# Kernel tuning notes

Hardware: AMD Instinct MI355X
Metric: run time of the kernel (lower is better)

The kernel has to match this reference:

```python
import jax, jax.numpy as jnp
import numpy as np

KH = KW = 3
PAD = 1
OFFG = 8  # offset groups: 144 offset channels / (2*9)


def conv2d(x, w, b, pad=PAD):
    out = jax.lax.conv_general_dilated(
        x, w, window_strides=(1, 1), padding=[(pad, pad), (pad, pad)],
        dimension_numbers=('NCHW', 'OIHW', 'NCHW'))
    return out + b[None, :, None, None]


def deform_conv2d(x, offset, w, b):
    # x: [B,C,H,W], offset: [B, 2*K*OFFG, H, W] (per group: (y,x) per kernel tap)
    B, C, H, W = x.shape
    K = KH * KW
    Cg = C // OFFG
    off = offset.reshape(B, OFFG, K, 2, H, W)
    ky, kx = jnp.meshgrid(jnp.arange(KH), jnp.arange(KW), indexing='ij')
    ky = ky.reshape(K).astype(x.dtype)
    kx = kx.reshape(K).astype(x.dtype)
    ys = (jnp.arange(H) - PAD).astype(x.dtype)  # stride 1, dilation 1
    xs = (jnp.arange(W) - PAD).astype(x.dtype)
    # sampling positions [B, OFFG, K, H, W]
    py = ys[None, None, None, :, None] + ky[None, None, :, None, None] + off[:, :, :, 0]
    px = xs[None, None, None, None, :] + kx[None, None, :, None, None] + off[:, :, :, 1]
    y0 = jnp.floor(py)
    x0 = jnp.floor(px)
    xg = x.reshape(B, OFFG, Cg, H * W)
    cols = jnp.zeros((B, OFFG, Cg, K, H, W), x.dtype)
    for dy in (0, 1):
        for dx in (0, 1):
            yi = y0 + dy
            xi = x0 + dx
            wgt = (1.0 - jnp.abs(py - yi)) * (1.0 - jnp.abs(px - xi))
            valid = (yi >= 0) & (yi < H) & (xi >= 0) & (xi < W)
            yc = jnp.clip(yi, 0, H - 1).astype(jnp.int32)
            xc = jnp.clip(xi, 0, W - 1).astype(jnp.int32)
            idx = (yc * W + xc).reshape(B, OFFG, 1, K * H * W)
            g = jnp.take_along_axis(xg, idx, axis=3).reshape(B, OFFG, Cg, K, H, W)
            cols = cols + g * (wgt * valid.astype(x.dtype))[:, :, None]
    cols = cols.reshape(B, C, K, H, W)
    out = jnp.einsum('bckhw,ock->bohw', cols, w.reshape(w.shape[0], C, K))
    return out + b[None, :, None, None]


def setup_inputs() -> dict:
    key = jax.random.key(0)
    ks = jax.random.split(key, 6)
    B, C, H, W = 16, 144, 64, 64
    feat_arm = jax.random.normal(ks[0], (B, C, H, W), jnp.float32)
    feat_up = jax.random.normal(ks[1], (B, C, H, W), jnp.float32)
    # offset conv: in=288 (cat), out=144 = 2*9*OFFG; small init so offsets are sane
    off_w = jax.random.normal(ks[2], (144, 288, 3, 3), jnp.float32) * 0.01
    off_b = jnp.zeros((144,), jnp.float32)
    dcn_w = jax.random.normal(ks[3], (256, 144, 3, 3), jnp.float32) * (1.0 / np.sqrt(144 * 9))
    dcn_b = jnp.zeros((256,), jnp.float32)
    return {'feat_arm': feat_arm, 'feat_up': feat_up, 'off_w': off_w,
            'off_b': off_b, 'dcn_w': dcn_w, 'dcn_b': dcn_b}


def reference(feat_arm, feat_up, off_w, off_b, dcn_w, dcn_b):
    x = jnp.concatenate([feat_arm, feat_up], axis=1)  # [B, 288, H, W]
    offset = conv2d(x, off_w, off_b)                  # [B, 144, H, W]
    y = deform_conv2d(feat_up, offset, dcn_w, dcn_b)  # [B, 256, H, W]
    return jax.nn.silu(y)
```

## Files before the change

### kernel.cpp

```cpp
#include <hip/hip_runtime.h>
#include <math.h>

constexpr int BN = 16;
constexpr int C_IN = 144, C_CAT = 288, C_OFF = 144, C_OUT = 256;
constexpr int OFFG = 8, CG = 18;

constexpr int FUB_ELEMS  = C_IN * BN * 4096;
constexpr int OFFP_ELEMS = BN * 72 * 4096;
constexpr int WOFF_PACK = 9 * 9 * 9 * 512;
constexpr int WDCN_PACK = 8 * 6 * 16 * 512;

typedef __attribute__((ext_vector_type(8))) short bf16x8;
typedef __attribute__((ext_vector_type(4))) float f32x4;
typedef __attribute__((ext_vector_type(2))) _Float16 f16x2;
typedef __attribute__((ext_vector_type(4))) unsigned u32x4;

__device__ __forceinline__ unsigned short f2bf(float f) {
  unsigned u = __builtin_bit_cast(unsigned, f);
  return (unsigned short)((u + 0x7FFFu + ((u >> 16) & 1u)) >> 16);
}

__device__ __forceinline__ unsigned packh2(float a, float b) {
  unsigned short ha = __builtin_bit_cast(unsigned short, (_Float16)a);
  unsigned short hb = __builtin_bit_cast(unsigned short, (_Float16)b);
  return (unsigned)ha | ((unsigned)hb << 16);
}
__device__ __forceinline__ float h2f_lo(unsigned u) {
  return (float)__builtin_bit_cast(_Float16, (unsigned short)(u & 0xFFFFu));
}
__device__ __forceinline__ float h2f_hi(unsigned u) {
  return (float)__builtin_bit_cast(_Float16, (unsigned short)(u >> 16));
}
__device__ __forceinline__ float bf_lo(unsigned u) {
  return __builtin_bit_cast(float, u << 16);
}
__device__ __forceinline__ float bf_hi(unsigned u) {
  return __builtin_bit_cast(float, u & 0xFFFF0000u);
}

__device__ __forceinline__ void gload_lds16(const void* g, void* l) {
  __builtin_amdgcn_global_load_lds(
      (const __attribute__((address_space(1))) unsigned*)g,
      (__attribute__((address_space(3))) unsigned*)l, 16, 0, 0);
}

__global__ __launch_bounds__(256) void tobf16_fu(
    const float* __restrict__ fu, unsigned short* __restrict__ fuB) {
  int i = (blockIdx.x * 256 + threadIdx.x) * 4;
  float4 v = *(const float4*)(fu + i);
  ushort4 o;
  o.x = f2bf(v.x); o.y = f2bf(v.y); o.z = f2bf(v.z); o.w = f2bf(v.w);
  *(ushort4*)(fuB + i) = o;
}

__global__ __launch_bounds__(256) void pack_w(
    const float* __restrict__ off_w, const float* __restrict__ dcn_w,
    unsigned short* __restrict__ wo, unsigned short* __restrict__ wd) {
  int idx = blockIdx.x * 256 + threadIdx.x;
  if (idx < WOFF_PACK) {
    int i = idx & 7, lane = (idx >> 3) & 63, t = idx >> 9;
    int mt = t % 9; t /= 9;
    int tap = t % 9, cb = t / 9;
    int co = mt * 16 + (lane & 15);
    int ci = cb * 32 + ((lane >> 4) << 3) + i;
    wo[idx] = f2bf(off_w[(co * C_CAT + ci) * 9 + tap]);
  }
  if (idx < WDCN_PACK) {
    int i = idx & 7, lane = (idx >> 3) & 63, t = idx >> 9;
    int mt = t & 15; t >>= 4;
    int ks = t % 6, g = t / 6;
    int co = mt * 16 + (lane & 15);
    int r = ks * 32 + ((lane >> 4) << 3) + i;
    float v = 0.f;
    if (r < 162) {
      int ci = r / 9, tap = r - ci * 9;
      v = dcn_w[(co * C_IN + g * CG + ci) * 9 + tap];
    }
    wd[idx] = f2bf(v);
  }
}

__global__ __launch_bounds__(256) void offs_conv_mfma(
    const float* __restrict__ fa, const float* __restrict__ fu,
    const unsigned short* __restrict__ wt, const float* __restrict__ bias,
    unsigned* __restrict__ offp) {
  const int b = blockIdx.x >> 5;
  const int y0 = (blockIdx.x & 31) << 1;
  const int tid = threadIdx.x;
  const int wave = tid >> 6, lane = tid & 63;
  const int kg = lane >> 4, ln = lane & 15;

  __shared__ __align__(16) unsigned short xs[4 * 66 * 32];

  f32x4 acc[9][2];
#pragma unroll
  for (int m = 0; m < 9; ++m)
#pragma unroll
    for (int n = 0; n < 2; ++n) acc[m][n] = {0.f, 0.f, 0.f, 0.f};

  for (int cb = 0; cb < 9; ++cb) {
    __syncthreads();
    for (int idx = tid; idx < 2112; idx += 256) {
      int q = idx / 264;
      int rem = idx - q * 264;
      int row = rem / 66;
      int cc = rem - row * 66;
      int y = y0 - 1 + row, x = cc - 1;
      ushort4 wv = make_ushort4(0, 0, 0, 0);
      if (y >= 0 && y < 64 && x >= 0 && x < 64) {
        int cib = cb * 32 + (q << 2);
        const float* p = (cib < C_IN)
                             ? fa + (((size_t)(b * C_IN + cib)) << 12)
                             : fu + (((size_t)(b * C_IN + cib - C_IN)) << 12);
        int o = (y << 6) + x;
        wv.x = f2bf(p[o]);
        wv.y = f2bf(p[o + 4096]);
        wv.z = f2bf(p[o + 8192]);
        wv.w = f2bf(p[o + 12288]);
      }
      int e = ((row * 66 + cc) << 5) + (((q >> 1) ^ (cc & 3)) << 3) + ((q & 1) << 2);
      *(ushort4*)&xs[e] = wv;
    }
    __syncthreads();

    for (int tap = 0; tap < 9; ++tap) {
      const int ky = tap / 3, kx = tap - ky * 3;
      bf16x8 a[9];
      const unsigned short* wp = wt + (((size_t)(cb * 9 + tap) * 9) << 9) + (lane << 3);
#pragma unroll
      for (int m = 0; m < 9; ++m) a[m] = *(const bf16x8*)(wp + (m << 9));
#pragma unroll
      for (int n = 0; n < 2; ++n) {
        int px = ((wave << 1) + n) * 16 + ln;
        int row = (px >> 6) + ky, cc = (px & 63) + kx;
        int e = ((row * 66 + cc) << 5) + ((kg ^ (cc & 3)) << 3);
        bf16x8 bv = *(const bf16x8*)&xs[e];
#pragma unroll
        for (int m = 0; m < 9; ++m)
          acc[m][n] = __builtin_amdgcn_mfma_f32_16x16x32_bf16(a[m], bv, acc[m][n], 0, 0, 0);
      }
    }
  }

#pragma unroll
  for (int n = 0; n < 2; ++n) {
    int px = ((wave << 1) + n) * 16 + ln;
    int y = y0 + (px >> 6), x = px & 63;
#pragma unroll
    for (int m = 0; m < 9; ++m) {
      int cob = m * 16 + (kg << 2);
#pragma unroll
      for (int rr = 0; rr < 4; rr += 2) {
        unsigned v = packh2(acc[m][n][rr] + bias[cob + rr],
                            acc[m][n][rr + 1] + bias[cob + rr + 1]);
        offp[(((size_t)(b * 72 + ((cob + rr) >> 1))) << 12) + (y << 6) + x] = v;
      }
    }
  }
}

__global__ __launch_bounds__(512, 4) void dcn_mfma(
    const unsigned short* __restrict__ fuB, const unsigned* __restrict__ offp,
    const unsigned short* __restrict__ wt, const float* __restrict__ bias,
    float* __restrict__ out) {
  const int b = blockIdx.x >> 6, h = blockIdx.x & 63;
  const int tid = threadIdx.x;
  const int wave = tid >> 6, lane = tid & 63;
  const int kg = lane >> 4, ln = lane & 15;
  const int wm = wave >> 2, wn = wave & 3;
  const int px = (wn << 4) + ln;

  __shared__ __align__(16) unsigned short colsT[64 * 202];
  __shared__ __align__(16) unsigned short wl[2][8192];

  f32x4 acc[8];
#pragma unroll
  for (int m = 0; m < 8; ++m) acc[m] = {0.f, 0.f, 0.f, 0.f};

  for (int i = tid; i < 64 * 15; i += 512) {
    int p = i / 15, d = i - p * 15;
    *(unsigned*)&colsT[p * 202 + 162 + 2 * d] = 0u;
  }

  {
    const unsigned short* src = wt + (wave * 2) * 512 + lane * 8;
#pragma unroll
    for (int j = 0; j < 2; ++j)
      gload_lds16(src + j * 512, &wl[0][(wave * 2 + j) * 512]);
  }

  auto make_geo = [&](int gg_, int tap, int p) -> uint4 {
    int ky = tap / 3, kx = tap - ky * 3;
    unsigned op = offp[(((size_t)(b * 72 + gg_ * 9 + tap)) << 12) + (h << 6) + p];
    float oy = h2f_lo(op), ox = h2f_hi(op);
    float py = (float)(h - 1 + ky) + oy;
    float pxs = (float)(p - 1 + kx) + ox;
    float y0f = floorf(py), x0f = floorf(pxs);
    int y0 = (int)y0f, x0 = (int)x0f;
    float fy = py - y0f, fx = pxs - x0f;
    float vy0 = (y0 >= 0 && y0 < 64) ? 1.f : 0.f;
    float vy1 = (y0 + 1 >= 0 && y0 + 1 < 64) ? 1.f : 0.f;
    float vx0 = (x0 >= 0 && x0 < 64) ? 1.f : 0.f;
    float vx1 = (x0 + 1 >= 0 && x0 + 1 < 64) ? 1.f : 0.f;
    float a0 = (1.f - fx) * vx0;
    float a1 = fx * vx1;
    float wlo = (x0 == -1) ? a1 : (x0 == 63 ? 0.f : a0);
    float whi = (x0 == 63) ? a0 : (x0 == -1 ? 0.f : a1);
    int xL = min(max(x0, 0), 62);
    int yc0 = min(max(y0, 0), 63), yc1 = min(max(y0 + 1, 0), 63);
    float cy0 = (1.f - fy) * vy0, cy1 = fy * vy1;
    uint4 r;
    r.x = (unsigned)((yc0 << 6) + xL) | ((unsigned)((yc1 << 6) + xL) << 16);
    r.y = 0u;
    r.z = packh2(cy0 * wlo, cy0 * whi);
    r.w = packh2(cy1 * wlo, cy1 * whi);
    return r;
  };

  int t = 0;
  for (int g = 0; g < OFFG; ++g) {
    __syncthreads();

    uint4 gg = make_geo(g, wave, lane);
    uint4 g8 = make_geo(g, 8, lane);

    const unsigned short* gbase = fuB + (((size_t)(b * C_IN + g * CG)) << 12);
    {
      const int iL0 = gg.x & 0xFFFFu, iL1 = gg.x >> 16;
      const float wl0 = h2f_lo(gg.z), wh0 = h2f_hi(gg.z);
      const float wl1 = h2f_lo(gg.w), wh1 = h2f_hi(gg.w);
      for (int cb = 0; cb < 18; cb += 6) {
        unsigned d0[6], d1[6];
#pragma unroll
        for (int u = 0; u < 6; ++u) {
          const unsigned short* pl = gbase + ((size_t)(cb + u) << 12);
          __builtin_memcpy(&d0[u], pl + iL0, 4);
          __builtin_memcpy(&d1[u], pl + iL1, 4);
        }
#pragma unroll
        for (int u = 0; u < 6; ++u) {
          float s = wl0 * bf_lo(d0[u]) + wh0 * bf_hi(d0[u]) +
                    wl1 * bf_lo(d1[u]) + wh1 * bf_hi(d1[u]);
          colsT[lane * 202 + (cb + u) * 9 + wave] = f2bf(s);
        }
      }
      const int j0 = g8.x & 0xFFFFu, j1 = g8.x >> 16;
      const float ul0 = h2f_lo(g8.z), uh0 = h2f_hi(g8.z);
      const float ul1 = h2f_lo(g8.w), uh1 = h2f_hi(g8.w);
      const int n8 = (wave < 2) ? 3 : 2;
      unsigned e0[3], e1[3];
#pragma unroll
      for (int u = 0; u < 3; ++u) {
        if (u < n8) {
          const unsigned short* pl = gbase + ((size_t)(wave + 8 * u) << 12);
          __builtin_memcpy(&e0[u], pl + j0, 4);
          __builtin_memcpy(&e1[u], pl + j1, 4);
        }
      }
#pragma unroll
      for (int u = 0; u < 3; ++u) {
        if (u < n8) {
          float s = ul0 * bf_lo(e0[u]) + uh0 * bf_hi(e0[u]) +
                    ul1 * bf_lo(e1[u]) + uh1 * bf_hi(e1[u]);
          colsT[lane * 202 + (wave + 8 * u) * 9 + 8] = f2bf(s);
        }
      }
    }
    __syncthreads();

    for (int ks = 0; ks < 6; ++ks, ++t) {
      int cbase = px * 202 + ks * 32 + (kg << 3);
      u32x4 bu;
      bu[0] = *(const unsigned*)&colsT[cbase];
      bu[1] = *(const unsigned*)&colsT[cbase + 2];
      bu[2] = *(const unsigned*)&colsT[cbase + 4];
      bu[3] = *(const unsigned*)&colsT[cbase + 6];
      bf16x8 bv = __builtin_bit_cast(bf16x8, bu);

      __syncthreads();

      if (t < 47) {
        const unsigned short* src =
            wt + (size_t)(t + 1) * 8192 + (wave * 2) * 512 + lane * 8;
        unsigned short* dst = wl[(t + 1) & 1];
#pragma unroll
        for (int j = 0; j < 2; ++j)
          gload_lds16(src + j * 512, dst + (wave * 2 + j) * 512);
      }

      const unsigned short* wbuf = wl[t & 1] + (wm * 8) * 512 + lane * 8;
#pragma unroll
      for (int j = 0; j < 8; ++j) {
        bf16x8 av = *(const bf16x8*)(wbuf + j * 512);
        acc[j] = __builtin_amdgcn_mfma_f32_16x16x32_bf16(av, bv, acc[j], 0, 0, 0);
      }
    }
  }

#pragma unroll
  for (int j = 0; j < 8; ++j) {
    int cob = (wm * 8 + j) * 16 + (kg << 2);
#pragma unroll
    for (int r = 0; r < 4; ++r) {
      float y = acc[j][r] + bias[cob + r];
      out[(((size_t)(b * C_OUT + cob + r)) << 12) + (h << 6) + px] =
          y / (1.f + expf(-y));
    }
  }
}

extern "C" void kernel_launch(void* const* d_in, const int* in_sizes, int n_in,
                              void* d_out, int out_size, void* d_ws, size_t ws_size,
                              hipStream_t stream) {
  const float* feat_arm = (const float*)d_in[0];
  const float* feat_up  = (const float*)d_in[1];
  const float* off_w    = (const float*)d_in[2];
  const float* off_b    = (const float*)d_in[3];
  const float* dcn_w    = (const float*)d_in[4];
  const float* dcn_b    = (const float*)d_in[5];
  float* out = (float*)d_out;

  unsigned short* fuB = (unsigned short*)d_ws;
  unsigned* offp = (unsigned*)(fuB + FUB_ELEMS);
  unsigned short* wo = (unsigned short*)(offp + OFFP_ELEMS);
  unsigned short* wd = wo + WOFF_PACK;

  tobf16_fu<<<FUB_ELEMS / 1024, 256, 0, stream>>>(feat_up, fuB);
  pack_w<<<(WDCN_PACK + 255) / 256, 256, 0, stream>>>(off_w, dcn_w, wo, wd);
  offs_conv_mfma<<<BN * 32, 256, 0, stream>>>(feat_arm, feat_up, wo, off_b, offp);
  dcn_mfma<<<BN * 64, 512, 0, stream>>>(fuB, offp, wd, dcn_b, out);
}
```

Baseline: 269.3 us.

## Load DCN weights directly from global memory instead of double-buffered LDS

After: 404.2 us. 50.1% more time.

```diff
diff --git a/kernel.cpp b/kernel.cpp
--- a/kernel.cpp
+++ b/kernel.cpp
@@ -12,7 +12,6 @@
 
 typedef __attribute__((ext_vector_type(8))) short bf16x8;
 typedef __attribute__((ext_vector_type(4))) float f32x4;
-typedef __attribute__((ext_vector_type(2))) _Float16 f16x2;
 typedef __attribute__((ext_vector_type(4))) unsigned u32x4;
 
 __device__ __forceinline__ unsigned short f2bf(float f) {
@@ -36,12 +35,6 @@
 }
 __device__ __forceinline__ float bf_hi(unsigned u) {
   return __builtin_bit_cast(float, u & 0xFFFF0000u);
-}
-
-__device__ __forceinline__ void gload_lds16(const void* g, void* l) {
-  __builtin_amdgcn_global_load_lds(
-      (const __attribute__((address_space(1))) unsigned*)g,
-      (__attribute__((address_space(3))) unsigned*)l, 16, 0, 0);
 }
 
 __global__ __launch_bounds__(256) void tobf16_fu(
@@ -159,7 +152,7 @@
   }
 }
 
-__global__ __launch_bounds__(512, 4) void dcn_mfma(
+__global__ __launch_bounds__(512, 6) void dcn_mfma(
     const unsigned short* __restrict__ fuB, const unsigned* __restrict__ offp,
     const unsigned short* __restrict__ wt, const float* __restrict__ bias,
     float* __restrict__ out) {
@@ -171,7 +164,6 @@
   const int px = (wn << 4) + ln;
 
   __shared__ __align__(16) unsigned short colsT[64 * 202];
-  __shared__ __align__(16) unsigned short wl[2][8192];
 
   f32x4 acc[8];
 #pragma unroll
@@ -180,13 +172,6 @@
   for (int i = tid; i < 64 * 15; i += 512) {
     int p = i / 15, d = i - p * 15;
     *(unsigned*)&colsT[p * 202 + 162 + 2 * d] = 0u;
-  }
-
-  {
-    const unsigned short* src = wt + (wave * 2) * 512 + lane * 8;
-#pragma unroll
-    for (int j = 0; j < 2; ++j)
-      gload_lds16(src + j * 512, &wl[0][(wave * 2 + j) * 512]);
   }
 
   auto make_geo = [&](int gg_, int tap, int p) -> uint4 {
@@ -217,7 +202,6 @@
     return r;
   };
 
-  int t = 0;
   for (int g = 0; g < OFFG; ++g) {
     __syncthreads();
 
@@ -268,7 +252,7 @@
     }
     __syncthreads();
 
-    for (int ks = 0; ks < 6; ++ks, ++t) {
+    for (int ks = 0; ks < 6; ++ks) {
       int cbase = px * 202 + ks * 32 + (kg << 3);
       u32x4 bu;
       bu[0] = *(const unsigned*)&colsT[cbase];
@@ -277,21 +261,11 @@
       bu[3] = *(const unsigned*)&colsT[cbase + 6];
       bf16x8 bv = __builtin_bit_cast(bf16x8, bu);
 
-      __syncthreads();
-
-      if (t < 47) {
-        const unsigned short* src =
-            wt + (size_t)(t + 1) * 8192 + (wave * 2) * 512 + lane * 8;
-        unsigned short* dst = wl[(t + 1) & 1];
-#pragma unroll
-        for (int j = 0; j < 2; ++j)
-          gload_lds16(src + j * 512, dst + (wave * 2 + j) * 512);
-      }
-
-      const unsigned short* wbuf = wl[t & 1] + (wm * 8) * 512 + lane * 8;
+      const unsigned short* wp =
+          wt + (size_t)(g * 6 + ks) * 8192 + (wm * 8) * 512 + lane * 8;
 #pragma unroll
       for (int j = 0; j < 8; ++j) {
-        bf16x8 av = *(const bf16x8*)(wbuf + j * 512);
+        bf16x8 av = *(const bf16x8*)(wp + j * 512);
         acc[j] = __builtin_amdgcn_mfma_f32_16x16x32_bf16(av, bv, acc[j], 0, 0, 0);
       }
     }
```

## Triple-buffer DCN weight tiles with vmcnt waits and merge prep kernels

Applied to the files above, without the earlier changes.

Measured after the change: 257.6 us. 1.05x faster.

```diff
diff --git a/kernel.cpp b/kernel.cpp
--- a/kernel.cpp
+++ b/kernel.cpp
@@ -12,7 +12,6 @@
 
 typedef __attribute__((ext_vector_type(8))) short bf16x8;
 typedef __attribute__((ext_vector_type(4))) float f32x4;
-typedef __attribute__((ext_vector_type(2))) _Float16 f16x2;
 typedef __attribute__((ext_vector_type(4))) unsigned u32x4;
 
 __device__ __forceinline__ unsigned short f2bf(float f) {
@@ -44,19 +43,18 @@
       (__attribute__((address_space(3))) unsigned*)l, 16, 0, 0);
 }
 
-__global__ __launch_bounds__(256) void tobf16_fu(
-    const float* __restrict__ fu, unsigned short* __restrict__ fuB) {
-  int i = (blockIdx.x * 256 + threadIdx.x) * 4;
-  float4 v = *(const float4*)(fu + i);
-  ushort4 o;
-  o.x = f2bf(v.x); o.y = f2bf(v.y); o.z = f2bf(v.z); o.w = f2bf(v.w);
-  *(ushort4*)(fuB + i) = o;
-}
-
-__global__ __launch_bounds__(256) void pack_w(
+__global__ __launch_bounds__(256) void prep(
+    const float* __restrict__ fu, unsigned short* __restrict__ fuB,
     const float* __restrict__ off_w, const float* __restrict__ dcn_w,
     unsigned short* __restrict__ wo, unsigned short* __restrict__ wd) {
   int idx = blockIdx.x * 256 + threadIdx.x;
+  int i4 = idx * 4;
+  if (i4 < FUB_ELEMS) {
+    float4 v = *(const float4*)(fu + i4);
+    ushort4 o;
+    o.x = f2bf(v.x); o.y = f2bf(v.y); o.z = f2bf(v.z); o.w = f2bf(v.w);
+    *(ushort4*)(fuB + i4) = o;
+  }
   if (idx < WOFF_PACK) {
     int i = idx & 7, lane = (idx >> 3) & 63, t = idx >> 9;
     int mt = t % 9; t /= 9;
@@ -171,7 +169,7 @@
   const int px = (wn << 4) + ln;
 
   __shared__ __align__(16) unsigned short colsT[64 * 202];
-  __shared__ __align__(16) unsigned short wl[2][8192];
+  __shared__ __align__(16) unsigned short wl[3][8192];
 
   f32x4 acc[8];
 #pragma unroll
@@ -217,7 +215,7 @@
     return r;
   };
 
-  int t = 0;
+  int tg = 0, cur = 0;
   for (int g = 0; g < OFFG; ++g) {
     __syncthreads();
 
@@ -268,7 +266,7 @@
     }
     __syncthreads();
 
-    for (int ks = 0; ks < 6; ++ks, ++t) {
+    for (int ks = 0; ks < 6; ++ks, ++tg) {
       int cbase = px * 202 + ks * 32 + (kg << 3);
       u32x4 bu;
       bu[0] = *(const unsigned*)&colsT[cbase];
@@ -277,23 +275,28 @@
       bu[3] = *(const unsigned*)&colsT[cbase + 6];
       bf16x8 bv = __builtin_bit_cast(bf16x8, bu);
 
-      __syncthreads();
-
-      if (t < 47) {
+      int nxt = cur + 1;
+      if (nxt == 3) nxt = 0;
+      if (tg < 47) {
         const unsigned short* src =
-            wt + (size_t)(t + 1) * 8192 + (wave * 2) * 512 + lane * 8;
-        unsigned short* dst = wl[(t + 1) & 1];
+            wt + (size_t)(tg + 1) * 8192 + (wave * 2) * 512 + lane * 8;
+        unsigned short* dst = wl[nxt];
 #pragma unroll
         for (int j = 0; j < 2; ++j)
           gload_lds16(src + j * 512, dst + (wave * 2 + j) * 512);
-      }
-
-      const unsigned short* wbuf = wl[t & 1] + (wm * 8) * 512 + lane * 8;
+        asm volatile("s_waitcnt vmcnt(2)" ::: "memory");
+      } else {
+        asm volatile("s_waitcnt vmcnt(0)" ::: "memory");
+      }
+      __builtin_amdgcn_s_barrier();
+
+      const unsigned short* wbuf = wl[cur] + (wm * 8) * 512 + lane * 8;
 #pragma unroll
       for (int j = 0; j < 8; ++j) {
         bf16x8 av = *(const bf16x8*)(wbuf + j * 512);
         acc[j] = __builtin_amdgcn_mfma_f32_16x16x32_bf16(av, bv, acc[j], 0, 0, 0);
       }
+      cur = nxt;
     }
   }
 
@@ -325,8 +328,7 @@
   unsigned short* wo = (unsigned short*)(offp + OFFP_ELEMS);
   unsigned short* wd = wo + WOFF_PACK;
 
-  tobf16_fu<<<FUB_ELEMS / 1024, 256, 0, stream>>>(feat_up, fuB);
-  pack_w<<<(WDCN_PACK + 255) / 256, 256, 0, stream>>>(off_w, dcn_w, wo, wd);
+  prep<<<FUB_ELEMS / 1024, 256, 0, stream>>>(feat_up, fuB, off_w, dcn_w, wo, wd);
   offs_conv_mfma<<<BN * 32, 256, 0, stream>>>(feat_arm, feat_up, wo, off_b, offp);
   dcn_mfma<<<BN * 64, 512, 0, stream>>>(fuB, offp, wd, dcn_b, out);
 }
```
